# Performance work log

Measured on AMD Instinct MI355X. Metric: run time of the kernel, lower is better.

## Reference

```python
import jax, jax.numpy as jnp
import numpy as np

EPS = 1e-6

def rms_norm(x, w):
    x32 = x.astype(jnp.float32)
    y = x32 * jax.lax.rsqrt(jnp.mean(x32 * x32, axis=-1, keepdims=True) + EPS)
    return y.astype(x.dtype) * w

def setup_inputs() -> dict:
    key = jax.random.key(0)
    ks = jax.random.split(key, 12)
    V, Dm, S, Bz, L = 32000, 1024, 256, 2, 2048
    input_ids = jax.random.randint(ks[0], (Bz, L), 0, V)
    embedding = 0.02 * jax.random.normal(ks[1], (V, Dm), dtype=jnp.float32)
    embed_norm_w = jnp.ones((Dm,), dtype=jnp.float32)
    ssm_norm_w = jnp.ones((Dm,), dtype=jnp.float32)
    # A = 0.999 * exp(1j * theta): magnitude 0.999, random phase
    theta = jax.random.normal(ks[2], (S,), dtype=jnp.float32)
    A_re = 0.999 * jnp.cos(theta)
    A_im = 0.999 * jnp.sin(theta)
    # complex randn has real/imag parts with std 1/sqrt(2)
    cs = 1.0 / np.sqrt(2.0)
    B_re = cs * jax.random.normal(ks[3], (Dm, S), dtype=jnp.float32) / np.sqrt(S)
    B_im = cs * jax.random.normal(ks[4], (Dm, S), dtype=jnp.float32) / np.sqrt(S)
    C_re = cs * jax.random.normal(ks[5], (S, Dm), dtype=jnp.float32) / np.sqrt(S)
    C_im = cs * jax.random.normal(ks[6], (S, Dm), dtype=jnp.float32) / np.sqrt(S)
    D_p = jax.random.normal(ks[7], (Dm,), dtype=jnp.float32)
    head_w = jax.random.normal(ks[8], (Dm, V), dtype=jnp.float32) / np.sqrt(Dm)
    head_b = jnp.zeros((V,), dtype=jnp.float32)
    return dict(input_ids=input_ids, embedding=embedding, embed_norm_w=embed_norm_w,
                ssm_norm_w=ssm_norm_w, A_re=A_re, A_im=A_im, B_re=B_re, B_im=B_im,
                C_re=C_re, C_im=C_im, D_p=D_p, head_w=head_w, head_b=head_b)

def reference(input_ids, embedding, embed_norm_w, ssm_norm_w, A_re, A_im,
              B_re, B_im, C_re, C_im, D_p, head_w, head_b):
    # embed + RMSNorm
    x = rms_norm(embedding[input_ids], embed_norm_w)      # [B, L, D]
    # SSM input norm
    u = rms_norm(x, ssm_norm_w)                           # [B, L, D]
    L = u.shape[1]
    A = (A_re + 1j * A_im).astype(jnp.complex64)          # [S]
    Bc = (B_re + 1j * B_im).astype(jnp.complex64)         # [D, S]
    Cc = (C_re + 1j * C_im).astype(jnp.complex64)         # [S, D]
    # per-channel geometric kernel A^t, t = 0..L-1
    t = jnp.arange(L)[:, None]
    A_powers = A[None, :] ** t                            # [L, S] complex64
    uB = jnp.einsum('bli,iz->blz', u.astype(jnp.complex64), Bc)  # [B, L, S]
    # FFT-based causal convolution (fast_conv)
    T = 1 << int(np.ceil(np.log2(2 * L - 1)))
    Af = jnp.fft.fft(A_powers, n=T, axis=0)               # [T, S]
    Uf = jnp.fft.fft(uB, n=T, axis=1)                     # [B, T, S]
    xs = jnp.fft.ifft(Af[None, :, :] * Uf, axis=1)[:, :L]  # [B, L, S]
    y = jnp.real(jnp.einsum('blz,zo->blo', xs, Cc)) + D_p  # [B, L, D]
    return y @ head_w + head_b                            # [B, L, V]
```

## Files before the change

### kernel.cpp

```cpp
#include <hip/hip_runtime.h>

static __device__ __forceinline__ unsigned short f2bf(float f) {
  union { float f; unsigned u; } v; v.f = f;
  unsigned r = v.u + 0x7fffu + ((v.u >> 16) & 1u);
  return (unsigned short)(r >> 16);
}

struct alignas(8) us4 { unsigned short x, y, z, w; };

typedef __bf16 bf16x8 __attribute__((ext_vector_type(8)));
typedef float f32x4 __attribute__((ext_vector_type(4)));

static __device__ __forceinline__ void load_lds16(const void* g, void* l) {
  __builtin_amdgcn_global_load_lds(
      (const __attribute__((address_space(1))) unsigned int*)g,
      (__attribute__((address_space(3))) unsigned int*)l,
      16, 0, 0);
}

static __device__ __forceinline__ float block_sum(float v, float* sred) {
  #pragma unroll
  for (int o = 32; o > 0; o >>= 1) v += __shfl_down(v, o, 64);
  const int tid = threadIdx.x;
  __syncthreads();
  if ((tid & 63) == 0) sred[tid >> 6] = v;
  __syncthreads();
  return sred[0] + sred[1] + sred[2] + sred[3];
}

__global__ __launch_bounds__(256) void embed_norm(
    const int* __restrict__ ids, const float* __restrict__ emb,
    const float* __restrict__ w1, const float* __restrict__ w2,
    unsigned short* __restrict__ u_bf)
{
  __shared__ float sred[4];
  const int row = blockIdx.x;
  const int tid = threadIdx.x;
  const int id = ids[row];
  const float4 e = *(const float4*)(emb + (size_t)id * 1024 + tid * 4);
  float tot = block_sum(e.x*e.x + e.y*e.y + e.z*e.z + e.w*e.w, sred);
  float inv1 = rsqrtf(tot * (1.0f/1024.0f) + 1e-6f);
  const float4 a = *(const float4*)(w1 + tid * 4);
  float x0 = e.x*inv1*a.x, x1 = e.y*inv1*a.y, x2 = e.z*inv1*a.z, x3 = e.w*inv1*a.w;
  float tot2 = block_sum(x0*x0 + x1*x1 + x2*x2 + x3*x3, sred);
  float inv2 = rsqrtf(tot2 * (1.0f/1024.0f) + 1e-6f);
  const float4 b = *(const float4*)(w2 + tid * 4);
  us4 o;
  o.x = f2bf(x0*inv2*b.x); o.y = f2bf(x1*inv2*b.y);
  o.z = f2bf(x2*inv2*b.z); o.w = f2bf(x3*inv2*b.w);
  *(us4*)(u_bf + (size_t)row * 1024 + tid * 4) = o;
}

__global__ __launch_bounds__(256) void pack_B(
    const float* __restrict__ B_re, const float* __restrict__ B_im,
    unsigned short* __restrict__ BT)
{
  int t = blockIdx.x * 256 + threadIdx.x;
  int n = t >> 10, k = t & 1023;
  float v = (n < 256) ? B_re[(size_t)k * 256 + n] : B_im[(size_t)k * 256 + (n - 256)];
  BT[t] = f2bf(v);
}

__global__ __launch_bounds__(256) void pack_C(
    const float* __restrict__ C_re, const float* __restrict__ C_im,
    unsigned short* __restrict__ CT)
{
  int t = blockIdx.x * 256 + threadIdx.x;
  int d = t >> 9, sc = t & 511;
  float v = (sc < 256) ? C_re[(size_t)sc * 1024 + d] : -C_im[(size_t)(sc - 256) * 1024 + d];
  CT[t] = f2bf(v);
}

__global__ __launch_bounds__(256) void transpose_cvt(
    const float* __restrict__ in, unsigned short* __restrict__ out, int Kd, int Nd)
{
  __shared__ float tile[32][33];
  const int n0 = blockIdx.x * 32, k0 = blockIdx.y * 32;
  const int tx = threadIdx.x, ty = threadIdx.y;
  #pragma unroll
  for (int j = 0; j < 32; j += 8)
    tile[ty + j][tx] = in[(size_t)(k0 + ty + j) * Nd + n0 + tx];
  __syncthreads();
  #pragma unroll
  for (int j = 0; j < 32; j += 8)
    out[(size_t)(n0 + ty + j) * Kd + k0 + tx] = f2bf(tile[tx][ty + j]);
}

template<bool OUT_BF16, bool HAS_BIAS>
__global__ __launch_bounds__(256) void gemm_bt(
    const unsigned short* __restrict__ A,
    const unsigned short* __restrict__ BT,
    const float* __restrict__ bias,
    void* __restrict__ outp,
    int M, int N, int K)
{
  __shared__ unsigned short As[128 * 32];
  __shared__ unsigned short Bs[128 * 32];
  const int tid = threadIdx.x;
  const int lane = tid & 63;
  const int wave = tid >> 6;
  const int m0 = blockIdx.y * 128;
  const int n0 = blockIdx.x * 128;
  const int wm = (wave >> 1) * 64;
  const int wn = (wave & 1) * 64;

  f32x4 acc[4][4] = {};

  const int lin0 = wave * 64 + lane;
  const int rowS = lin0 >> 2;
  const int koS = (lin0 & 3) * 8;
  const int aq = lane >> 4;
  const int al = lane & 15;

  for (int k0 = 0; k0 < K; k0 += 32) {
    load_lds16(A  + (size_t)(m0 + rowS)      * K + k0 + koS, As + (size_t)lin0 * 8);
    load_lds16(A  + (size_t)(m0 + 64 + rowS) * K + k0 + koS, As + (size_t)(256 + lin0) * 8);
    load_lds16(BT + (size_t)(n0 + rowS)      * K + k0 + koS, Bs + (size_t)lin0 * 8);
    load_lds16(BT + (size_t)(n0 + 64 + rowS) * K + k0 + koS, Bs + (size_t)(256 + lin0) * 8);
    __syncthreads();
    const bf16x8* Ap = (const bf16x8*)As;
    const bf16x8* Bp = (const bf16x8*)Bs;
    bf16x8 af[4], bfr[4];
    #pragma unroll
    for (int i = 0; i < 4; ++i) af[i] = Ap[(wm + i * 16 + al) * 4 + aq];
    #pragma unroll
    for (int j = 0; j < 4; ++j) bfr[j] = Bp[(wn + j * 16 + al) * 4 + aq];
    #pragma unroll
    for (int i = 0; i < 4; ++i)
      #pragma unroll
      for (int j = 0; j < 4; ++j)
        acc[i][j] = __builtin_amdgcn_mfma_f32_16x16x32_bf16(af[i], bfr[j], acc[i][j], 0, 0, 0);
    __syncthreads();
  }

  const int row0 = m0 + wm + (lane >> 4) * 4;
  const int col0 = n0 + wn + al;
  #pragma unroll
  for (int j = 0; j < 4; ++j) {
    const int col = col0 + j * 16;
    float bv = 0.f;
    if (HAS_BIAS) bv = bias[col];
    #pragma unroll
    for (int i = 0; i < 4; ++i) {
      #pragma unroll
      for (int r = 0; r < 4; ++r) {
        float v = acc[i][j][r] + bv;
        size_t o = (size_t)(row0 + i * 16 + r) * N + col;
        if (OUT_BF16) ((unsigned short*)outp)[o] = f2bf(v);
        else          ((float*)outp)[o] = v;
      }
    }
  }
}

__global__ __launch_bounds__(256) void local_scan(
    float* __restrict__ xs, float* __restrict__ carry,
    const float* __restrict__ A_re, const float* __restrict__ A_im)
{
  int t = blockIdx.x * 256 + threadIdx.x;
  int s = t & 255;
  int chunk = (t >> 8) & 15;
  int b = t >> 12;
  float ar = A_re[s], ai = A_im[s];
  float xr = 0.f, xi = 0.f;
  size_t base = ((size_t)(b * 2048 + chunk * 128)) * 512 + s;
  for (int j = 0; j < 128; ++j) {
    float ur = xs[base], ui = xs[base + 256];
    float nr = fmaf(ar, xr, fmaf(-ai, xi, ur));
    float ni = fmaf(ar, xi, fmaf(ai, xr, ui));
    xs[base] = nr; xs[base + 256] = ni;
    xr = nr; xi = ni;
    base += 512;
  }
  int ci = (b * 16 + chunk) * 512 + s;
  carry[ci] = xr; carry[ci + 256] = xi;
}

__global__ __launch_bounds__(256) void carry_scan(
    const float* __restrict__ A_re, const float* __restrict__ A_im,
    const float* __restrict__ carry, float* __restrict__ state_before,
    float* __restrict__ Apow)
{
  int s = threadIdx.x;
  float ar = A_re[s], ai = A_im[s];
  float pr = 1.f, pi = 0.f;
  for (int t = 0; t <= 128; ++t) {
    Apow[t * 512 + s] = pr; Apow[t * 512 + 256 + s] = pi;
    float nr = pr * ar - pi * ai;
    float ni = pr * ai + pi * ar;
    pr = nr; pi = ni;
  }
  float cr = Apow[128 * 512 + s], ci = Apow[128 * 512 + 256 + s];
  for (int b = 0; b < 2; ++b) {
    float str = 0.f, sti = 0.f;
    for (int c = 0; c < 16; ++c) {
      int idx = (b * 16 + c) * 512 + s;
      state_before[idx] = str; state_before[idx + 256] = sti;
      float lr = carry[idx], li = carry[idx + 256];
      float nr = lr + cr * str - ci * sti;
      float ni = li + cr * sti + ci * str;
      str = nr; sti = ni;
    }
  }
}

__global__ __launch_bounds__(256) void combine_cast(
    const float* __restrict__ xs, const float* __restrict__ state_before,
    const float* __restrict__ Apow, unsigned short* __restrict__ xs_cat)
{
  int t = blockIdx.x * 256 + threadIdx.x;
  int s = t & 255, row = t >> 8;
  int l = row & 2047, b = row >> 11;
  int chunk = l >> 7, j = l & 127;
  size_t o = (size_t)row * 512 + s;
  float xr = xs[o], xi = xs[o + 256];
  int sbi = (b * 16 + chunk) * 512 + s;
  float sr = state_before[sbi], si = state_before[sbi + 256];
  int api = (j + 1) * 512 + s;
  float pr = Apow[api], pi = Apow[api + 256];
  float fr = xr + pr * sr - pi * si;
  float fi = xi + pr * si + pi * sr;
  xs_cat[o] = f2bf(fr); xs_cat[o + 256] = f2bf(fi);
}

extern "C" void kernel_launch(void* const* d_in, const int* in_sizes, int n_in,
                              void* d_out, int out_size, void* d_ws, size_t ws_size,
                              hipStream_t stream) {
  (void)in_sizes; (void)n_in; (void)out_size; (void)ws_size;
  const int*   ids    = (const int*)d_in[0];
  const float* emb    = (const float*)d_in[1];
  const float* w1     = (const float*)d_in[2];
  const float* w2     = (const float*)d_in[3];
  const float* A_re   = (const float*)d_in[4];
  const float* A_im   = (const float*)d_in[5];
  const float* B_re   = (const float*)d_in[6];
  const float* B_im   = (const float*)d_in[7];
  const float* C_re   = (const float*)d_in[8];
  const float* C_im   = (const float*)d_in[9];
  const float* D_p    = (const float*)d_in[10];
  const float* head_w = (const float*)d_in[11];
  const float* head_b = (const float*)d_in[12];
  float* out = (float*)d_out;

  char* ob = (char*)d_out;
  unsigned short* u_bf   = (unsigned short*)(ob + 0);
  unsigned short* BcatT  = (unsigned short*)(ob + 8388608);
  float* uBxs            = (float*)(ob + 9437184);
  float* carry           = (float*)(ob + 17825792);
  float* state_before    = (float*)(ob + 17891328);
  float* Apow            = (float*)(ob + 17956864);
  unsigned short* xs_cat = (unsigned short*)(ob + 18221056);
  unsigned short* CcatT  = (unsigned short*)(ob + 22415360);

  char* wb = (char*)d_ws;
  unsigned short* head_wT = (unsigned short*)(wb + 0);
  unsigned short* y_bf    = (unsigned short*)(wb + 65536000);

  embed_norm<<<4096, 256, 0, stream>>>(ids, emb, w1, w2, u_bf);
  pack_B<<<2048, 256, 0, stream>>>(B_re, B_im, BcatT);
  pack_C<<<2048, 256, 0, stream>>>(C_re, C_im, CcatT);
  transpose_cvt<<<dim3(1000, 32), dim3(32, 8), 0, stream>>>(head_w, head_wT, 1024, 32000);

  gemm_bt<false, false><<<dim3(4, 32), 256, 0, stream>>>(u_bf, BcatT, nullptr, uBxs, 4096, 512, 1024);

  local_scan<<<32, 256, 0, stream>>>(uBxs, carry, A_re, A_im);
  carry_scan<<<1, 256, 0, stream>>>(A_re, A_im, carry, state_before, Apow);
  combine_cast<<<4096, 256, 0, stream>>>(uBxs, state_before, Apow, xs_cat);

  gemm_bt<true, true><<<dim3(8, 32), 256, 0, stream>>>(xs_cat, CcatT, D_p, y_bf, 4096, 1024, 512);

  gemm_bt<false, true><<<dim3(250, 32), 256, 0, stream>>>(y_bf, head_wT, head_b, out, 4096, 32000, 1024);
}
```

Measured before the change: 1.107 ms.

## Remap GEMM tiles per XCD for L2 locality and use nontemporal output stores

Switches the GEMM grid to 1D and remaps block IDs so consecutive tiles assigned to the same XCD share N-columns (M-fastest ordering), improving L2 reuse of the B operand within each XCD. Adds a template option for nontemporal stores on the large fp32 logits output to avoid polluting cache. The remap assumes M divisible by 128 and adds a little index arithmetic per block.

After: 1.084 ms. 2.1% less time.

```diff
diff --git a/kernel.cpp b/kernel.cpp
--- a/kernel.cpp
+++ b/kernel.cpp
@@ -86,7 +86,7 @@
     out[(size_t)(n0 + ty + j) * Kd + k0 + tx] = f2bf(tile[tx][ty + j]);
 }
 
-template<bool OUT_BF16, bool HAS_BIAS>
+template<bool OUT_BF16, bool HAS_BIAS, bool NT_STORE>
 __global__ __launch_bounds__(256) void gemm_bt(
     const unsigned short* __restrict__ A,
     const unsigned short* __restrict__ BT,
@@ -99,8 +99,18 @@
   const int tid = threadIdx.x;
   const int lane = tid & 63;
   const int wave = tid >> 6;
-  const int m0 = blockIdx.y * 128;
-  const int n0 = blockIdx.x * 128;
+
+  const int nwg = gridDim.x;
+  const int bid = blockIdx.x;
+  const int q = nwg >> 3, r = nwg & 7;
+  const int xcd = bid & 7, loc = bid >> 3;
+  const int g = (xcd < r ? xcd * (q + 1) : r * (q + 1) + (xcd - r) * q) + loc;
+  const int nMt = M >> 7;
+  const int mt = g % nMt;
+  const int nt = g / nMt;
+  const int m0 = mt << 7;
+  const int n0 = nt << 7;
+
   const int wm = (wave >> 1) * 64;
   const int wn = (wave & 1) * 64;
 
@@ -143,11 +153,16 @@
     #pragma unroll
     for (int i = 0; i < 4; ++i) {
       #pragma unroll
-      for (int r = 0; r < 4; ++r) {
-        float v = acc[i][j][r] + bv;
-        size_t o = (size_t)(row0 + i * 16 + r) * N + col;
-        if (OUT_BF16) ((unsigned short*)outp)[o] = f2bf(v);
-        else          ((float*)outp)[o] = v;
+      for (int r2 = 0; r2 < 4; ++r2) {
+        float v = acc[i][j][r2] + bv;
+        size_t o = (size_t)(row0 + i * 16 + r2) * N + col;
+        if (OUT_BF16) {
+          ((unsigned short*)outp)[o] = f2bf(v);
+        } else if (NT_STORE) {
+          __builtin_nontemporal_store(v, (float*)outp + o);
+        } else {
+          ((float*)outp)[o] = v;
+        }
       }
     }
   }
@@ -261,13 +276,13 @@
   pack_C<<<2048, 256, 0, stream>>>(C_re, C_im, CcatT);
   transpose_cvt<<<dim3(1000, 32), dim3(32, 8), 0, stream>>>(head_w, head_wT, 1024, 32000);
 
-  gemm_bt<false, false><<<dim3(4, 32), 256, 0, stream>>>(u_bf, BcatT, nullptr, uBxs, 4096, 512, 1024);
+  gemm_bt<false, false, false><<<128, 256, 0, stream>>>(u_bf, BcatT, nullptr, uBxs, 4096, 512, 1024);
 
   local_scan<<<32, 256, 0, stream>>>(uBxs, carry, A_re, A_im);
   carry_scan<<<1, 256, 0, stream>>>(A_re, A_im, carry, state_before, Apow);
   combine_cast<<<4096, 256, 0, stream>>>(uBxs, state_before, Apow, xs_cat);
 
-  gemm_bt<true, true><<<dim3(8, 32), 256, 0, stream>>>(xs_cat, CcatT, D_p, y_bf, 4096, 1024, 512);
-
-  gemm_bt<false, true><<<dim3(250, 32), 256, 0, stream>>>(y_bf, head_wT, head_b, out, 4096, 32000, 1024);
-}
+  gemm_bt<true, true, false><<<256, 256, 0, stream>>>(xs_cat, CcatT, D_p, y_bf, 4096, 1024, 512);
+
+  gemm_bt<false, true, true><<<8000, 256, 0, stream>>>(y_bf, head_wT, head_b, out, 4096, 32000, 1024);
+}
```
